# Performance work log

Hardware: AMD Instinct MI355X
Metric: run time of the kernel (lower is better)

Reference implementation:

```python
import jax, jax.numpy as jnp
import numpy as np


def setup_inputs() -> dict:
    key = jax.random.key(0)
    k1, k2 = jax.random.split(key)
    B, C, H, W = 64, 2, 512, 512
    inp = jax.random.normal(k1, (B, C, H, W), dtype=jnp.float32)
    tgt = jax.random.uniform(k2, (B, C, H, W), dtype=jnp.float32)
    return {"input": inp, "target": tgt}


def reference(input, target):
    B, C, H, W = input.shape
    # coordinate maps: x_map[:, j] = (j+1)/W, y_map[p, :] = (p+1)/H
    x_map = (jnp.arange(W, dtype=input.dtype) + 1.0) / W  # (W,)
    y_map = (jnp.arange(H, dtype=input.dtype) + 1.0) / H  # (H,)

    # DSNT soft-argmax: softmax over flattened H*W per (batch, keypoint)
    p = jax.nn.softmax(input.reshape(B, C, H * W), axis=-1).reshape(B, C, H, W)
    pred_x = jnp.einsum('bchw,w->bc', p, x_map)  # normalized coords
    pred_y = jnp.einsum('bchw,h->bc', p, y_map)

    # ground truth via flat argmax (matches torch.argmax on the 2D map)
    am = jnp.argmax(target.reshape(B, C, H * W), axis=-1)  # (B, C) int
    true_x = ((am % W) + 1).astype(input.dtype) / W
    true_y = ((am // W) + 1).astype(input.dtype) / H

    # convert normalized coords to pixel coords
    pred_xp, pred_yp = pred_x * W, pred_y * H
    true_xp, true_yp = true_x * W, true_y * H

    x_diff = true_xp - pred_xp  # (B, C)
    y_diff = true_yp - pred_yp

    s_x = jnp.sum(jnp.sqrt(x_diff ** 2)).reshape(1)
    s_y = jnp.sum(jnp.sqrt(y_diff ** 2)).reshape(1)

    ed = jnp.sqrt(x_diff ** 2 + y_diff ** 2)  # (B, C) per-point pixel ED
    s_i = jnp.sum(ed[:, 0]).reshape(1)          # keypoint o == 0
    s_s = jnp.sum(ed[:, 1:]).reshape(1)         # keypoints o > 0
    tot_list = jnp.sum(ed, axis=1)              # (B,)

    # diameter: distance between keypoint 0 and keypoint 1
    vpx, vpy = pred_xp[:, 0] - pred_xp[:, 1], pred_yp[:, 0] - pred_yp[:, 1]
    vtx, vty = true_xp[:, 0] - true_xp[:, 1], true_yp[:, 0] - true_yp[:, 1]
    pred_dist = jnp.sqrt(vpx ** 2 + vpy ** 2)
    true_dist = jnp.sqrt(vtx ** 2 + vty ** 2)
    diam_list = jnp.sqrt((pred_dist - true_dist) ** 2)  # (B,)
    s_diam = jnp.sum(diam_list).reshape(1)

    return (s_i, s_s, s_i + s_s, s_diam, tot_list, diam_list, s_x, s_y, B)
```

## Files before the change

kernel.cpp:

```cpp
#include <hip/hip_runtime.h>
#include <math.h>
#include <float.h>


namespace {
constexpr int S_SPLIT = 16;
constexpr int PAIRS   = 128;
constexpr int HW      = 512 * 512;
constexpr int CHUNK4  = HW / 4 / S_SPLIT;

typedef float f4 __attribute__((ext_vector_type(4)));

struct Partial {
    float l, sx, sy, tval;
    int   tidx;
    int   pad0, pad1, pad2;
};
}

__global__ __launch_bounds__(256, 4) void dsnt_partial(
        const float* __restrict__ inp,
        const float* __restrict__ tgt,
        Partial* __restrict__ part) {
    const int blk   = blockIdx.x;
    const int pair  = blk >> 4;
    const int split = blk & (S_SPLIT - 1);
    const int tid   = threadIdx.x;
    const f4* in4 = reinterpret_cast<const f4*>(inp + (size_t)pair * HW) + split * CHUNK4;
    const f4* tg4 = reinterpret_cast<const f4*>(tgt + (size_t)pair * HW) + split * CHUNK4;
    const int base4 = split * CHUNK4;
    const float inv = 1.0f / 512.0f;

    const int w0 = (tid * 4) & 511;
    const float fx0 = (float)(w0 + 1) * inv;
    const float fx1 = (float)(w0 + 2) * inv;
    const float fx2 = (float)(w0 + 3) * inv;
    const float fx3 = (float)(w0 + 4) * inv;
    const int rowbase0 = split * 32 + (tid >> 7);

    float l = 0.f, sx = 0.f, sy = 0.f;
    float tv = -1.0f;
    int   ti = 0;

    auto acc = [&](f4 x, f4 t, float fy, int idx) {
        const float e0 = __expf(x.x);
        const float e1 = __expf(x.y);
        const float e2 = __expf(x.z);
        const float e3 = __expf(x.w);
        const float es = (e0 + e1) + (e2 + e3);
        l += es;
        sy = fmaf(es, fy, sy);
        sx = fmaf(e0, fx0, fmaf(e1, fx1, fmaf(e2, fx2, fmaf(e3, fx3, sx))));
        bool g;
        g = t.x > tv; tv = g ? t.x : tv; ti = g ? idx     : ti;
        g = t.y > tv; tv = g ? t.y : tv; ti = g ? idx + 1 : ti;
        g = t.z > tv; tv = g ? t.z : tv; ti = g ? idx + 2 : ti;
        g = t.w > tv; tv = g ? t.w : tv; ti = g ? idx + 3 : ti;
    };

    #pragma unroll
    for (int s = 0; s < 4; ++s) {
        const int i0 = tid + s * 1024;
        const f4 x0 = __builtin_nontemporal_load(&in4[i0]);
        const f4 x1 = __builtin_nontemporal_load(&in4[i0 + 256]);
        const f4 x2 = __builtin_nontemporal_load(&in4[i0 + 512]);
        const f4 x3 = __builtin_nontemporal_load(&in4[i0 + 768]);
        const f4 t0 = __builtin_nontemporal_load(&tg4[i0]);
        const f4 t1 = __builtin_nontemporal_load(&tg4[i0 + 256]);
        const f4 t2 = __builtin_nontemporal_load(&tg4[i0 + 512]);
        const f4 t3 = __builtin_nontemporal_load(&tg4[i0 + 768]);

        const int rb = rowbase0 + 8 * s;
        acc(x0, t0, (float)(rb + 1) * inv, (base4 + i0) * 4);
        acc(x1, t1, (float)(rb + 3) * inv, (base4 + i0 + 256) * 4);
        acc(x2, t2, (float)(rb + 5) * inv, (base4 + i0 + 512) * 4);
        acc(x3, t3, (float)(rb + 7) * inv, (base4 + i0 + 768) * 4);
    }

    for (int off = 32; off > 0; off >>= 1) {
        l  += __shfl_down(l,  off);
        sx += __shfl_down(sx, off);
        sy += __shfl_down(sy, off);
        const float ov = __shfl_down(tv, off);
        const int   oi = __shfl_down(ti, off);
        if (ov > tv || (ov == tv && oi < ti)) { tv = ov; ti = oi; }
    }

    __shared__ float sl[4], ssx[4], ssy[4], stv[4];
    __shared__ int   sti[4];
    const int wid  = tid >> 6;
    const int lane = tid & 63;
    if (lane == 0) { sl[wid] = l; ssx[wid] = sx; ssy[wid] = sy; stv[wid] = tv; sti[wid] = ti; }
    __syncthreads();

    if (tid == 0) {
        float L = 0.f, SX = 0.f, SY = 0.f, TV = -1.0f;
        int TI = 0x7fffffff;
        #pragma unroll
        for (int w = 0; w < 4; ++w) {
            L += sl[w]; SX += ssx[w]; SY += ssy[w];
            if (stv[w] > TV || (stv[w] == TV && sti[w] < TI)) { TV = stv[w]; TI = sti[w]; }
        }
        Partial p;
        p.l = L; p.sx = SX; p.sy = SY; p.tval = TV; p.tidx = TI;
        p.pad0 = p.pad1 = p.pad2 = 0;
        part[blk] = p;
    }
}

__global__ __launch_bounds__(1024) void dsnt_final(
        const Partial* __restrict__ part,
        float* __restrict__ out, int out_size) {
    __shared__ float pxp[PAIRS], pyp[PAIRS], txp[PAIRS], typ[PAIRS];
    __shared__ float edl[PAIRS], axl[PAIRS], ayl[PAIRS];
    const int tid = threadIdx.x;

    const Partial a = part[2 * tid];
    const Partial b = part[2 * tid + 1];
    float L = a.l + b.l, SX = a.sx + b.sx, SY = a.sy + b.sy;
    float tv = a.tval; int ti = a.tidx;
    if (b.tval > tv || (b.tval == tv && b.tidx < ti)) { tv = b.tval; ti = b.tidx; }

    #pragma unroll
    for (int off = 1; off < 8; off <<= 1) {
        L  += __shfl_xor(L,  off);
        SX += __shfl_xor(SX, off);
        SY += __shfl_xor(SY, off);
        const float ov = __shfl_xor(tv, off);
        const int   oi = __shfl_xor(ti, off);
        if (ov > tv || (ov == tv && oi < ti)) { tv = ov; ti = oi; }
    }

    if ((tid & 7) == 0) {
        const int p = tid >> 3;
        const float px = SX / L * 512.0f;
        const float py = SY / L * 512.0f;
        const float tx = (float)((ti & 511) + 1);
        const float ty = (float)((ti >> 9) + 1);
        const float xd = tx - px, yd = ty - py;
        pxp[p] = px; pyp[p] = py; txp[p] = tx; typ[p] = ty;
        edl[p] = sqrtf(xd * xd + yd * yd);
        axl[p] = fabsf(xd);
        ayl[p] = fabsf(yd);
    }
    __syncthreads();

    if (tid < 64) {
        const int bb = tid;
        const float e0 = edl[2 * bb], e1 = edl[2 * bb + 1];
        out[4 + bb] = e0 + e1;
        const float vpx = pxp[2 * bb] - pxp[2 * bb + 1], vpy = pyp[2 * bb] - pyp[2 * bb + 1];
        const float vtx = txp[2 * bb] - txp[2 * bb + 1], vty = typ[2 * bb] - typ[2 * bb + 1];
        const float pd = sqrtf(vpx * vpx + vpy * vpy);
        const float td = sqrtf(vtx * vtx + vty * vty);
        const float diam = fabsf(pd - td);
        out[68 + bb] = diam;

        float si = e0, ss = e1, sd = diam;
        float sxs = axl[2 * bb] + axl[2 * bb + 1];
        float sys = ayl[2 * bb] + ayl[2 * bb + 1];
        #pragma unroll
        for (int off = 32; off > 0; off >>= 1) {
            si  += __shfl_xor(si,  off);
            ss  += __shfl_xor(ss,  off);
            sd  += __shfl_xor(sd,  off);
            sxs += __shfl_xor(sxs, off);
            sys += __shfl_xor(sys, off);
        }
        if (tid == 0) {
            out[0] = si;
            out[1] = ss;
            out[2] = si + ss;
            out[3] = sd;
            out[132] = sxs;
            out[133] = sys;
            if (out_size >= 135) out[134] = 64.0f;
        }
    }
}

extern "C" void kernel_launch(void* const* d_in, const int* in_sizes, int n_in,
                              void* d_out, int out_size, void* d_ws, size_t ws_size,
                              hipStream_t stream) {
    const float* inp = (const float*)d_in[0];
    const float* tgt = (const float*)d_in[1];
    float* out = (float*)d_out;
    Partial* part = (Partial*)d_ws;

    dsnt_partial<<<PAIRS * S_SPLIT, 256, 0, stream>>>(inp, tgt, part);
    dsnt_final<<<1, 1024, 0, stream>>>(part, out, out_size);
}
```

Baseline: 253.0 us.

## Split softmax-moment and argmax work into separate block kinds

Each chunk is now handled by two blocks: even blocks stream only the input and accumulate the softmax sums and coordinate moments, while odd blocks stream only the target and compute the argmax. The grid doubles, launch bounds allow more resident blocks, and each thread issues eight loads per batch. The aim is more memory-level parallelism and lower register pressure in this bandwidth-bound reduction. The cost is twice as many blocks and per-block reductions, plus a second partial array the final kernel reads.

```diff
diff --git a/kernel.cpp b/kernel.cpp
--- a/kernel.cpp
+++ b/kernel.cpp
@@ -8,118 +8,134 @@
 constexpr int PAIRS   = 128;
 constexpr int HW      = 512 * 512;
 constexpr int CHUNK4  = HW / 4 / S_SPLIT;
+constexpr int UNITS   = PAIRS * S_SPLIT;
 
 typedef float f4 __attribute__((ext_vector_type(4)));
 
-struct Partial {
-    float l, sx, sy, tval;
-    int   tidx;
-    int   pad0, pad1, pad2;
-};
-}
-
-__global__ __launch_bounds__(256, 4) void dsnt_partial(
+struct SmP { float l, sx, sy, pad; };
+struct AmP { float tv; int ti; };
+}
+
+__global__ __launch_bounds__(256, 8) void dsnt_partial(
         const float* __restrict__ inp,
         const float* __restrict__ tgt,
-        Partial* __restrict__ part) {
+        SmP* __restrict__ smp,
+        AmP* __restrict__ amp) {
     const int blk   = blockIdx.x;
-    const int pair  = blk >> 4;
-    const int split = blk & (S_SPLIT - 1);
+    const int kind  = blk & 1;
+    const int unit  = blk >> 1;
+    const int pair  = unit >> 4;
+    const int split = unit & (S_SPLIT - 1);
     const int tid   = threadIdx.x;
-    const f4* in4 = reinterpret_cast<const f4*>(inp + (size_t)pair * HW) + split * CHUNK4;
-    const f4* tg4 = reinterpret_cast<const f4*>(tgt + (size_t)pair * HW) + split * CHUNK4;
+    const int lane  = tid & 63;
+    const int wid   = tid >> 6;
     const int base4 = split * CHUNK4;
     const float inv = 1.0f / 512.0f;
 
-    const int w0 = (tid * 4) & 511;
-    const float fx0 = (float)(w0 + 1) * inv;
-    const float fx1 = (float)(w0 + 2) * inv;
-    const float fx2 = (float)(w0 + 3) * inv;
-    const float fx3 = (float)(w0 + 4) * inv;
-    const int rowbase0 = split * 32 + (tid >> 7);
-
-    float l = 0.f, sx = 0.f, sy = 0.f;
-    float tv = -1.0f;
-    int   ti = 0;
-
-    auto acc = [&](f4 x, f4 t, float fy, int idx) {
-        const float e0 = __expf(x.x);
-        const float e1 = __expf(x.y);
-        const float e2 = __expf(x.z);
-        const float e3 = __expf(x.w);
-        const float es = (e0 + e1) + (e2 + e3);
-        l += es;
-        sy = fmaf(es, fy, sy);
-        sx = fmaf(e0, fx0, fmaf(e1, fx1, fmaf(e2, fx2, fmaf(e3, fx3, sx))));
-        bool g;
-        g = t.x > tv; tv = g ? t.x : tv; ti = g ? idx     : ti;
-        g = t.y > tv; tv = g ? t.y : tv; ti = g ? idx + 1 : ti;
-        g = t.z > tv; tv = g ? t.z : tv; ti = g ? idx + 2 : ti;
-        g = t.w > tv; tv = g ? t.w : tv; ti = g ? idx + 3 : ti;
-    };
-
-    #pragma unroll
-    for (int s = 0; s < 4; ++s) {
-        const int i0 = tid + s * 1024;
-        const f4 x0 = __builtin_nontemporal_load(&in4[i0]);
-        const f4 x1 = __builtin_nontemporal_load(&in4[i0 + 256]);
-        const f4 x2 = __builtin_nontemporal_load(&in4[i0 + 512]);
-        const f4 x3 = __builtin_nontemporal_load(&in4[i0 + 768]);
-        const f4 t0 = __builtin_nontemporal_load(&tg4[i0]);
-        const f4 t1 = __builtin_nontemporal_load(&tg4[i0 + 256]);
-        const f4 t2 = __builtin_nontemporal_load(&tg4[i0 + 512]);
-        const f4 t3 = __builtin_nontemporal_load(&tg4[i0 + 768]);
-
-        const int rb = rowbase0 + 8 * s;
-        acc(x0, t0, (float)(rb + 1) * inv, (base4 + i0) * 4);
-        acc(x1, t1, (float)(rb + 3) * inv, (base4 + i0 + 256) * 4);
-        acc(x2, t2, (float)(rb + 5) * inv, (base4 + i0 + 512) * 4);
-        acc(x3, t3, (float)(rb + 7) * inv, (base4 + i0 + 768) * 4);
-    }
-
-    for (int off = 32; off > 0; off >>= 1) {
-        l  += __shfl_down(l,  off);
-        sx += __shfl_down(sx, off);
-        sy += __shfl_down(sy, off);
-        const float ov = __shfl_down(tv, off);
-        const int   oi = __shfl_down(ti, off);
-        if (ov > tv || (ov == tv && oi < ti)) { tv = ov; ti = oi; }
-    }
-
-    __shared__ float sl[4], ssx[4], ssy[4], stv[4];
-    __shared__ int   sti[4];
-    const int wid  = tid >> 6;
-    const int lane = tid & 63;
-    if (lane == 0) { sl[wid] = l; ssx[wid] = sx; ssy[wid] = sy; stv[wid] = tv; sti[wid] = ti; }
-    __syncthreads();
-
-    if (tid == 0) {
-        float L = 0.f, SX = 0.f, SY = 0.f, TV = -1.0f;
-        int TI = 0x7fffffff;
-        #pragma unroll
-        for (int w = 0; w < 4; ++w) {
-            L += sl[w]; SX += ssx[w]; SY += ssy[w];
-            if (stv[w] > TV || (stv[w] == TV && sti[w] < TI)) { TV = stv[w]; TI = sti[w]; }
-        }
-        Partial p;
-        p.l = L; p.sx = SX; p.sy = SY; p.tval = TV; p.tidx = TI;
-        p.pad0 = p.pad1 = p.pad2 = 0;
-        part[blk] = p;
+    __shared__ float sh0[4], sh1[4], sh2[4];
+    __shared__ int   sh3[4];
+
+    if (kind == 0) {
+        const f4* in4 = reinterpret_cast<const f4*>(inp + (size_t)pair * HW) + base4;
+        const int w0 = (tid * 4) & 511;
+        const float fx0 = (float)(w0 + 1) * inv;
+        const float fx1 = (float)(w0 + 2) * inv;
+        const float fx2 = (float)(w0 + 3) * inv;
+        const float fx3 = (float)(w0 + 4) * inv;
+        const int rowbase0 = split * 32 + (tid >> 7);
+
+        float l = 0.f, sx = 0.f, sy = 0.f;
+        #pragma unroll
+        for (int s = 0; s < 2; ++s) {
+            const int i0 = tid + s * 2048;
+            f4 x[8];
+            #pragma unroll
+            for (int c = 0; c < 8; ++c)
+                x[c] = __builtin_nontemporal_load(&in4[i0 + c * 256]);
+            const int rb = rowbase0 + 16 * s;
+            #pragma unroll
+            for (int c = 0; c < 8; ++c) {
+                const float fy = (float)(rb + 2 * c + 1) * inv;
+                const float e0 = __expf(x[c].x);
+                const float e1 = __expf(x[c].y);
+                const float e2 = __expf(x[c].z);
+                const float e3 = __expf(x[c].w);
+                const float es = (e0 + e1) + (e2 + e3);
+                l += es;
+                sy = fmaf(es, fy, sy);
+                sx = fmaf(e0, fx0, fmaf(e1, fx1, fmaf(e2, fx2, fmaf(e3, fx3, sx))));
+            }
+        }
+        #pragma unroll
+        for (int off = 32; off > 0; off >>= 1) {
+            l  += __shfl_down(l,  off);
+            sx += __shfl_down(sx, off);
+            sy += __shfl_down(sy, off);
+        }
+        if (lane == 0) { sh0[wid] = l; sh1[wid] = sx; sh2[wid] = sy; }
+        __syncthreads();
+        if (tid == 0) {
+            float L = 0.f, SX = 0.f, SY = 0.f;
+            #pragma unroll
+            for (int w = 0; w < 4; ++w) { L += sh0[w]; SX += sh1[w]; SY += sh2[w]; }
+            SmP p; p.l = L; p.sx = SX; p.sy = SY; p.pad = 0.f;
+            smp[unit] = p;
+        }
+    } else {
+        const f4* tg4 = reinterpret_cast<const f4*>(tgt + (size_t)pair * HW) + base4;
+        float tv = -1.0f;
+        int   ti = 0;
+        #pragma unroll
+        for (int s = 0; s < 2; ++s) {
+            const int i0 = tid + s * 2048;
+            f4 t[8];
+            #pragma unroll
+            for (int c = 0; c < 8; ++c)
+                t[c] = __builtin_nontemporal_load(&tg4[i0 + c * 256]);
+            #pragma unroll
+            for (int c = 0; c < 8; ++c) {
+                const int idx = (base4 + i0 + c * 256) * 4;
+                bool g;
+                g = t[c].x > tv; tv = g ? t[c].x : tv; ti = g ? idx     : ti;
+                g = t[c].y > tv; tv = g ? t[c].y : tv; ti = g ? idx + 1 : ti;
+                g = t[c].z > tv; tv = g ? t[c].z : tv; ti = g ? idx + 2 : ti;
+                g = t[c].w > tv; tv = g ? t[c].w : tv; ti = g ? idx + 3 : ti;
+            }
+        }
+        #pragma unroll
+        for (int off = 32; off > 0; off >>= 1) {
+            const float ov = __shfl_down(tv, off);
+            const int   oi = __shfl_down(ti, off);
+            if (ov > tv || (ov == tv && oi < ti)) { tv = ov; ti = oi; }
+        }
+        if (lane == 0) { sh0[wid] = tv; sh3[wid] = ti; }
+        __syncthreads();
+        if (tid == 0) {
+            float TV = -1.0f; int TI = 0x7fffffff;
+            #pragma unroll
+            for (int w = 0; w < 4; ++w)
+                if (sh0[w] > TV || (sh0[w] == TV && sh3[w] < TI)) { TV = sh0[w]; TI = sh3[w]; }
+            AmP p; p.tv = TV; p.ti = TI;
+            amp[unit] = p;
+        }
     }
 }
 
 __global__ __launch_bounds__(1024) void dsnt_final(
-        const Partial* __restrict__ part,
+        const SmP* __restrict__ smp,
+        const AmP* __restrict__ amp,
         float* __restrict__ out, int out_size) {
     __shared__ float pxp[PAIRS], pyp[PAIRS], txp[PAIRS], typ[PAIRS];
     __shared__ float edl[PAIRS], axl[PAIRS], ayl[PAIRS];
     const int tid = threadIdx.x;
 
-    const Partial a = part[2 * tid];
-    const Partial b = part[2 * tid + 1];
+    const SmP a  = smp[2 * tid];
+    const SmP b  = smp[2 * tid + 1];
+    const AmP a2 = amp[2 * tid];
+    const AmP b2 = amp[2 * tid + 1];
     float L = a.l + b.l, SX = a.sx + b.sx, SY = a.sy + b.sy;
-    float tv = a.tval; int ti = a.tidx;
-    if (b.tval > tv || (b.tval == tv && b.tidx < ti)) { tv = b.tval; ti = b.tidx; }
+    float tv = a2.tv; int ti = a2.ti;
+    if (b2.tv > tv || (b2.tv == tv && b2.ti < ti)) { tv = b2.tv; ti = b2.ti; }
 
     #pragma unroll
     for (int off = 1; off < 8; off <<= 1) {
@@ -185,8 +201,9 @@
     const float* inp = (const float*)d_in[0];
     const float* tgt = (const float*)d_in[1];
     float* out = (float*)d_out;
-    Partial* part = (Partial*)d_ws;
-
-    dsnt_partial<<<PAIRS * S_SPLIT, 256, 0, stream>>>(inp, tgt, part);
-    dsnt_final<<<1, 1024, 0, stream>>>(part, out, out_size);
-}
+    SmP* smp = (SmP*)d_ws;
+    AmP* amp = (AmP*)((char*)d_ws + UNITS * sizeof(SmP));
+
+    dsnt_partial<<<UNITS * 2, 256, 0, stream>>>(inp, tgt, smp, amp);
+    dsnt_final<<<1, 1024, 0, stream>>>(smp, amp, out, out_size);
+}
```

Measured after the change: 251.0 us (median of 2 runs). Within noise of the previous version (-0.8%).
